# Kernel optimization log

Measured on AMD Instinct MI355X. Metric: run time of the kernel, lower is better.

Reference implementation:

```python
import jax, jax.numpy as jnp
import numpy as np

H = W = 256
L = H * W                      # number of graph vertices / tree leaves
N_NODES = 2 * L - 1            # binary partition tree node count
LAM = 1.0                      # lambda_ (soft-area temperature)


def _grid_edges():
    """4-adjacency grid graph edges (same structure as higra get_4_adjacency_graph)."""
    idx = np.arange(L, dtype=np.int64).reshape(H, W)
    src = np.concatenate([idx[:, :-1].ravel(), idx[:-1, :].ravel()])
    dst = np.concatenate([idx[:, 1:].ravel(), idx[1:, :].ravel()])
    return src.astype(np.int32), dst.astype(np.int32)


def setup_inputs() -> dict:
    key = jax.random.key(0)
    src, dst = _grid_edges()
    ew = jax.random.uniform(key, (src.shape[0],), dtype=jnp.float32)
    return {"edge_weights": ew,
            "edges_src": jnp.asarray(src),
            "edges_dst": jnp.asarray(dst)}


def _build_tree(ew, src, dst):
    """higra.bpt_canonical: Kruskal over stably-sorted edges, building a binary
    merge tree. Leaves are 0..L-1, internal node L+i is created by the i-th MST
    edge. Returns (sizes, mst_edge_map, ancestor paths). All integer structure
    is piecewise-constant w.r.t. edge_weights (no gradient flows through it)."""
    order = np.argsort(ew, kind="stable")
    uf = np.arange(L)

    def find(x):
        r = x
        while uf[r] != r:
            r = uf[r]
        while uf[x] != r:
            uf[x], x = r, uf[x]
        return r

    canon = np.arange(L)                      # tree node of each union-find root
    parent = np.arange(N_NODES)               # self-parent until set (root keeps self)
    sizes = np.ones(N_NODES, dtype=np.float32)
    edge_map = np.zeros(L - 1, dtype=np.int64)
    node = L
    for ei in order:
        a = find(src[ei]); b = find(dst[ei])
        if a == b:
            continue
        na, nb = canon[a], canon[b]
        parent[na] = node
        parent[nb] = node
        sizes[node] = sizes[na] + sizes[nb]
        edge_map[node - L] = ei
        uf[a] = b
        canon[b] = node
        node += 1
    # self-inclusive ancestor paths, padded by repeating the root
    cur = np.arange(N_NODES)
    cols = [cur.copy()]
    while np.any(parent[cur] != cur):
        cur = parent[cur]
        cols.append(cur.copy())
    paths = np.stack(cols, axis=1)            # [N_NODES, D+1]
    return sizes, edge_map, paths


def _softarea(edge_weights, edge_map, sizes_np, paths_np):
    """Soft area of every tree node n:
       area(n) = sum_x sigmoid((alt(n) - d(x, n)) / lambda)
    where d(x,n) is the min ultrametric distance from leaf x to the leaves of n:
      - x in subtree(n), x != n : d = alt(parent(x))
      - x == n (leaf)           : d = 0
      - x outside subtree(n)    : d = alt(lowest ancestor of n containing x).
    Outside leaves are grouped per ancestor a (count = size(a) - size(previous
    node on the path)), giving an O(N * depth) vectorized computation."""
    alt = jnp.concatenate([jnp.zeros((L,), edge_weights.dtype),
                           edge_weights[edge_map]])          # [N_NODES]
    alt_path = alt[paths_np]                                  # [N, D+1]
    size_path = sizes_np[paths_np]                            # constant, numpy
    diff = jnp.asarray(size_path[:, 1:] - size_path[:, :-1])  # 0 on root padding
    outside = jnp.sum(
        diff * jax.nn.sigmoid((alt[:, None] - alt_path[:, 1:]) / LAM), axis=1)

    # inside: each leaf x contributes sigmoid((alt(a_k) - alt(parent(x)))/lam)
    # to every proper ancestor a_k, plus sigmoid(0)=0.5 to itself (alt(leaf)=0).
    lp = paths_np[:L]                                         # [L, D+1]
    alt_lp = alt_path[:L]
    valid = jnp.asarray((lp[:, 1:] != lp[:, :-1]).astype(np.float32))
    vals = jax.nn.sigmoid((alt_lp[:, 1:] - alt_lp[:, 1:2]) / LAM) * valid
    inside = jax.ops.segment_sum(vals.reshape(-1),
                                 jnp.asarray(lp[:, 1:].reshape(-1)),
                                 num_segments=N_NODES)
    inside = inside.at[:L].add(0.5)
    return inside + outside


def reference(edge_weights, edges_src, edges_dst):
    sizes, edge_map, paths = _build_tree(np.asarray(edge_weights),
                                         np.asarray(edges_src),
                                         np.asarray(edges_dst))
    return _softarea(edge_weights, jnp.asarray(edge_map), sizes, paths)
```

## Files before the change

kernel.cpp:

```cpp
#include <hip/hip_runtime.h>
#include <stdint.h>

typedef unsigned int u32;
typedef unsigned short u16;

#define L_VERTS 65536
#define N_EDGES 130560
#define N_NODES 131071
#define NODEPAD 131072

#define CCH 170
#define SCH 768
#define MAXSV 1536
#define HSZ 2048

#define NB 255
#define TPB 64
#define IPT 8
#define IPB 512

__global__ void init_keys(const float* __restrict__ w, u32* __restrict__ keys, u32* __restrict__ vals,
                          u32* szG, u16* canonTop16, u32* parent, float* alt){
  int i = blockIdx.x*blockDim.x + threadIdx.x;
  if(i < N_EDGES){ keys[i] = __float_as_uint(w[i]); vals[i] = (u32)i; }
  if(i < N_NODES){ parent[i]=(u32)i; alt[i]=0.f; }
  if(i < L_VERTS){ szG[i]=1u; canonTop16[i]=0xFFFFu; }
}

__global__ void radix_hist(const u32* __restrict__ idx, const u32* __restrict__ keys,
                           u32* __restrict__ histG, int shift){
  __shared__ u32 h[256];
  for(int i=threadIdx.x;i<256;i+=TPB) h[i]=0;
  __syncthreads();
  int base = blockIdx.x*IPB + threadIdx.x*IPT;
  #pragma unroll
  for(int i=0;i<IPT;i++){
    u32 e = idx[base+i];
    u32 d = (keys[e]>>shift)&255u;
    atomicAdd(&h[d],1u);
  }
  __syncthreads();
  for(int i=threadIdx.x;i<256;i+=TPB) histG[i*NB+blockIdx.x]=h[i];
}

__global__ void radix_scan(u32* histG){
  const int M = 256*NB;
  __shared__ u32 sums[1024];
  int t=threadIdx.x; int s=t*64; u32 acc=0;
  for(int i=0;i<64;i++){int id=s+i; if(id<M) acc+=histG[id];}
  sums[t]=acc; __syncthreads();
  for(int off=1; off<1024; off<<=1){
    u32 v=(t>=off)?sums[t-off]:0u;
    __syncthreads();
    sums[t]+=v;
    __syncthreads();
  }
  u32 run = (t==0)?0u:sums[t-1];
  for(int i=0;i<64;i++){int id=s+i; if(id<M){u32 v=histG[id]; histG[id]=run; run+=v;}}
}

__global__ void radix_scatter(const u32* __restrict__ idxIn, const u32* __restrict__ keys,
                              u32* __restrict__ idxOut, const u32* __restrict__ histG, int shift){
  __shared__ u16 thoff[256][TPB];
  int t=threadIdx.x;
  for(int d=t;d<256;d+=TPB) for(int j=0;j<TPB;j++) thoff[d][j]=0;
  __syncthreads();
  int base = blockIdx.x*IPB + t*IPT;
  u32 myv[IPT]; u32 myd[IPT];
  #pragma unroll
  for(int i=0;i<IPT;i++){
    myv[i]=idxIn[base+i];
    myd[i]=(keys[myv[i]]>>shift)&255u;
    thoff[myd[i]][t]++;
  }
  __syncthreads();
  for(int dd=0;dd<4;dd++){
    int d=t*4+dd; u32 run=0;
    for(int j=0;j<TPB;j++){ u32 v=thoff[d][j]; thoff[d][j]=(u16)run; run+=v; }
  }
  __syncthreads();
  #pragma unroll
  for(int i=0;i<IPT;i++){
    u32 d=myd[i];
    u32 pos = histG[d*NB+blockIdx.x] + (u32)thoff[d][t];
    thoff[d][t]++;
    idxOut[pos]=myv[i];
  }
}

__global__ void build_epair(const u32* __restrict__ order, const int* __restrict__ srcv,
                            const int* __restrict__ dstv, u32* __restrict__ epair){
  int p=blockIdx.x*blockDim.x+threadIdx.x;
  if(p>=N_EDGES) return;
  u32 e=order[p];
  epair[p]=((u32)dstv[e]<<16)|(u32)srcv[e];
}

__device__ __forceinline__ u32 ald(u32* p){
  return __hip_atomic_load(p, __ATOMIC_RELAXED, __HIP_MEMORY_SCOPE_AGENT);
}
__device__ __forceinline__ void ast(u32* p, u32 v){
  __hip_atomic_store(p, v, __ATOMIC_RELAXED, __HIP_MEMORY_SCOPE_AGENT);
}

__global__ void __launch_bounds__(1024,1) p1_checkpoints(
    const u32* __restrict__ epair,
    u32* szG, u16* lid16, u16* svroot16, u16* svsize16, u16* svnext16, u32* mG)
{
  __shared__ u16 ufL[L_VERTS];
  __shared__ u32 hkey[HSZ];
  __shared__ u32 sufL[MAXSV];
  __shared__ u32 compsz[MAXSV];
  __shared__ u32 repkey[MAXSV];
  __shared__ u16 lidL[2*SCH];
  __shared__ u32 mcnt;
  int t = threadIdx.x;
  for(int i=t;i<L_VERTS/2;i+=1024) ((u32*)ufL)[i]=((2u*(u32)i+1u)<<16)|(2u*(u32)i);
  for(int k=0;k<CCH;k++){
    for(int i=t;i<HSZ;i+=1024) hkey[i]=0xFFFFFFFFu;
    for(u32 s=t;s<MAXSV;s+=1024){ sufL[s]=s; compsz[s]=0u; repkey[s]=0u; }
    if(t==0) mcnt=0u;
    __syncthreads();
    int base = k*SCH;
    for(int i=t;i<2*SCH;i+=1024){
      u32 pr = epair[base+(i>>1)];
      u32 v = (i&1)? (pr>>16) : (pr&0xFFFFu);
      u32 x=v;
      while(true){ u32 px=ufL[x]; if(px==x)break; u32 g=ufL[px]; if(g!=px) ufL[x]=(u16)g; x=g; }
      u32 r=x;
      if(v!=r) ufL[v]=(u16)r;
      u32 h=(r*2654435761u)>>21;
      while(true){
        u32 old=atomicCAS(&hkey[h],0xFFFFFFFFu,(r<<16)|0x7FFFu);
        if(old==0xFFFFFFFFu){
          u32 id=atomicAdd(&mcnt,1u);
          svroot16[k*MAXSV+id]=(u16)r;
          hkey[h]=(r<<16)|id;
          break;
        }
        if((old>>16)==r) break;
        h=(h+1)&(HSZ-1u);
      }
      lidL[i]=(u16)h;
    }
    __syncthreads();
    u32 mc=mcnt;
    if(t==0) mG[k]=mc;
    for(u32 s=t;s<mc;s+=1024){
      u32 r=(u32)svroot16[k*MAXSV+s];
      svsize16[k*MAXSV+s]=(u16)(ald(&szG[r])-1u);
    }
    for(int i=t;i<2*SCH;i+=1024) lid16[2*base+i]=(u16)(hkey[lidL[i]]&0xFFFFu);
    for(int j=t;j<SCH;j+=1024){
      u32 sa=hkey[lidL[2*j]]&0xFFFFu, sb=hkey[lidL[2*j+1]]&0xFFFFu;
      if(sa==sb) continue;
      while(true){
        u32 x=sa; while(true){u32 p2=sufL[x]; if(p2==x)break; u32 g=sufL[p2]; if(g!=p2) sufL[x]=g; x=g;}
        u32 y=sb; while(true){u32 p2=sufL[y]; if(p2==y)break; u32 g=sufL[p2]; if(g!=p2) sufL[y]=g; y=g;}
        if(x==y) break;
        u32 hi=x>y?x:y, lo=x^y^hi;
        if(atomicCAS(&sufL[hi],hi,lo)==hi) break;
        sa=hi; sb=lo;
      }
    }
    __syncthreads();
    for(u32 s=t;s<mc;s+=1024){
      u32 x=s; while(true){u32 p2=sufL[x]; if(p2==x)break; x=p2;}
      sufL[s]=x;
      u32 sz=(u32)svsize16[k*MAXSV+s]+1u;
      atomicAdd(&compsz[x], sz);
      atomicMax(&repkey[x], (sz<<11) | (2047u-s));
    }
    __syncthreads();
    for(u32 s=t;s<mc;s+=1024){
      u32 rs=sufL[s];
      u32 rep=2047u-(repkey[rs]&2047u);
      u32 wv=(u32)svroot16[k*MAXSV+rep];
      svnext16[k*MAXSV+s]=(u16)wv;
      u32 myroot=(u32)svroot16[k*MAXSV+s];
      if(myroot!=wv) ufL[myroot]=(u16)wv;
      if(s==rep)     ast(&szG[wv], compsz[rs]);
    }
    __syncthreads();
  }
}

__global__ void __launch_bounds__(64) p2_chunk(
  const u16* __restrict__ lid16,
  const u16* __restrict__ svsize16, const u16* __restrict__ svnext16, const u32* __restrict__ mG,
  u16* __restrict__ outChA, u16* __restrict__ outChB, u16* __restrict__ outSize16, u16* __restrict__ outJ16,
  u32* __restrict__ accCnt, u16* __restrict__ compR16, u16* __restrict__ compTop16, u32* __restrict__ ncomp)
{
  int k = blockIdx.x; int t = threadIdx.x;
  __shared__ u16 uf[MAXSV];
  __shared__ u32 csize[MAXSV];
  __shared__ u16 ctop[MAXSV];
  __shared__ u16 svnl[MAXSV];
  __shared__ u32 lidP[SCH];
  __shared__ u32 cmp_s;
  u32 m = mG[k];
  int base=k*SCH;
  for(u32 s=t;s<m;s+=64){
    uf[s]=(u16)s;
    csize[s]=(u32)svsize16[k*MAXSV+s]+1u;
    ctop[s]=(u16)s;
    svnl[s]=svnext16[k*MAXSV+s];
  }
  for(int j=t;j<SCH;j+=64) lidP[j]=((const u32*)lid16)[base+j];
  if(t==0) cmp_s=0u;
  __syncthreads();
  if(t==0){
    u32 cnt=0;
    for(int j=0;j<SCH;j++){
      u32 lw = lidP[j];
      u32 la = lw & 0xFFFFu, lb = lw >> 16;
      u32 x=la; while(true){u32 px=uf[x]; if(px==x)break; u32 g=uf[px]; uf[x]=(u16)g; x=g;}
      u32 y=lb; while(true){u32 py=uf[y]; if(py==y)break; u32 g=uf[py]; uf[y]=(u16)g; y=g;}
      if(x==y) continue;
      u32 sa=csize[x], sb=csize[y], ns=sa+sb;
      outChA[base+cnt]=ctop[x];
      outChB[base+cnt]=ctop[y];
      outSize16[base+cnt]=(u16)(ns-1u);
      outJ16[base+cnt]=(u16)j;
      u32 win=(sa>=sb)?x:y, los=x^y^win;
      uf[los]=(u16)win; csize[win]=ns; ctop[win]=(u16)(0x8000u|cnt);
      cnt++;
    }
    accCnt[k]=cnt;
  }
  __syncthreads();
  for(u32 s=t;s<m;s+=64){
    if(uf[s]==(u16)s && (ctop[s]&0x8000u)){
      u32 pos=atomicAdd(&cmp_s,1u);
      compR16[k*MAXSV+pos]=svnl[s];
      compTop16[k*MAXSV+pos]=(u16)(ctop[s]&0x7FFFu);
    }
  }
  __syncthreads();
  if(t==0) ncomp[k]=cmp_s;
}

__global__ void __launch_bounds__(1024) p3_stitch(
  const u32* __restrict__ accCnt, const u16* __restrict__ outChA, const u16* __restrict__ outChB,
  const u16* __restrict__ outSize16, const u16* __restrict__ outJ16,
  const u16* __restrict__ svroot16,
  const u16* __restrict__ compR16, const u16* __restrict__ compTop16, const u32* __restrict__ ncomp,
  const u32* __restrict__ order, const float* __restrict__ w,
  u16* __restrict__ canonTop16, u32* __restrict__ parent, float* __restrict__ alt, u16* __restrict__ usize16)
{
  __shared__ u32 accBase[CCH];
  int t=threadIdx.x;
  if(t==0){ u32 r=0; for(int k=0;k<CCH;k++){ accBase[k]=r; r+=accCnt[k]; } }
  __syncthreads();
  for(int idx=t; idx<N_EDGES; idx+=1024){
    int k = idx/SCH; int j = idx - k*SCH;
    if(j < (int)accCnt[k]){
      u32 nid = (u32)L_VERTS + accBase[k] + (u32)j;
      u32 p = (u32)(k*SCH) + (u32)outJ16[idx];
      alt[nid] = w[order[p]];
      usize16[nid] = outSize16[idx];
      u32 cA=outChA[idx]; if(cA & 0x8000u) parent[(u32)L_VERTS+accBase[k]+(cA&0x7FFFu)] = nid;
      u32 cB=outChB[idx]; if(cB & 0x8000u) parent[(u32)L_VERTS+accBase[k]+(cB&0x7FFFu)] = nid;
    }
  }
  __syncthreads();
  for(int k=0;k<CCH;k++){
    u32 ac=accCnt[k];
    for(u32 j=t;j<ac;j+=1024){
      u32 idx=(u32)(k*SCH)+j;
      u32 nid=(u32)L_VERTS+accBase[k]+j;
      u32 cA=outChA[idx];
      if(!(cA&0x8000u)){
        u32 root=(u32)svroot16[k*MAXSV+cA];
        u32 ct=(u32)canonTop16[root];
        parent[(ct==0xFFFFu)?root:((u32)L_VERTS+ct)]=nid;
      }
      u32 cB=outChB[idx];
      if(!(cB&0x8000u)){
        u32 root=(u32)svroot16[k*MAXSV+cB];
        u32 ct=(u32)canonTop16[root];
        parent[(ct==0xFFFFu)?root:((u32)L_VERTS+ct)]=nid;
      }
    }
    __syncthreads();
    u32 nc=ncomp[k];
    for(u32 j=t;j<nc;j+=1024){
      canonTop16[(u32)compR16[k*MAXSV+j]] = (u16)(accBase[k]+compTop16[k*MAXSV+j]);
    }
    __syncthreads();
  }
}

__device__ __forceinline__ void hvals6(float v, float* o){
  float v2=v*v, v3=v2*v, v4=v2*v2, v5=v4*v;
  o[0]=0.5f-0.25f*v+v3*(1.f/48.f)-v5*(1.f/480.f);
  o[1]=0.25f-v2*(1.f/16.f)+v4*(1.f/96.f);
  o[2]=v*(1.f/16.f)-v3*(1.f/48.f);
  o[3]=v2*(1.f/48.f)-(1.f/48.f);
  o[4]=-v*(1.f/96.f);
  o[5]=(1.f/480.f);
}

__global__ void zero_both(u32* cc, float* nodeM, u32* ctr){
  int i=blockIdx.x*blockDim.x+threadIdx.x;
  if(i<L_VERTS) cc[i]=0u;
  if(i<6*NODEPAD) nodeM[i]=0.f;
  if(i==0) *ctr=0u;
}

__global__ void prep_init(const u32* __restrict__ parent, const u16* __restrict__ usize16,
                          u32* cc, u32* J0, uint2* A0, float* out){
  int n=blockIdx.x*blockDim.x+threadIdx.x;
  if(n>=N_NODES) return;
  out[n] = (n<L_VERTS)?0.5f:0.0f;
  if(n==N_NODES-1){ J0[n]=(u32)n; A0[n]=make_uint2(0u,0u); return; }
  u32 p=parent[n];
  u32 ord=atomicAdd(&cc[p-L_VERTS],1u);
  u32 szP=(u32)usize16[p]+1u;
  u32 szN=(n<L_VERTS)?1u:((u32)usize16[n]+1u);
  u32 sib=szP-szN;
  A0[n]=make_uint2(ord? sib:0u, 1u + (ord? (2u*sib-1u):0u));
  J0[n]=p;
}

__global__ void triple_round(const u32* __restrict__ Jin, const uint2* __restrict__ Ain,
                             u32* __restrict__ Jout, uint2* __restrict__ Aout){
  int n=blockIdx.x*blockDim.x+threadIdx.x;
  if(n>=N_NODES) return;
  u32 j1=Jin[n], j2=Jin[j1], j3=Jin[j2], j4=Jin[j3], j5=Jin[j4], j6=Jin[j5], j7=Jin[j6];
  uint2 a0=Ain[n], a1=Ain[j1], a2=Ain[j2], a3=Ain[j3], a4=Ain[j4], a5=Ain[j5], a6=Ain[j6], a7=Ain[j7];
  Aout[n]=make_uint2(a0.x+a1.x+a2.x+a3.x+a4.x+a5.x+a6.x+a7.x,
                     a0.y+a1.y+a2.y+a3.y+a4.y+a5.y+a6.y+a7.y);
  Jout[n]=Jin[j7];
}

__global__ void scatter_all(const u32* __restrict__ parent, const float* __restrict__ alt,
                            const u16* __restrict__ usize16, const uint2* __restrict__ accF,
                            float* __restrict__ leafM, float* __restrict__ nodeM){
  int n=blockIdx.x*blockDim.x+threadIdx.x;
  if(n>=N_NODES) return;
  u32 p=parent[n];
  float h[6]; hvals6(alt[p],h);
  uint2 af=accF[n];
  if(n<L_VERTS){
    u32 pos=af.x;
    #pragma unroll
    for(int j=0;j<6;j++) leafM[(size_t)j*L_VERTS+pos]=h[j];
  }
  if(n<N_NODES-1){
    u32 szP=(u32)usize16[p]+1u;
    u32 szN=(n<L_VERTS)?1u:((u32)usize16[n]+1u);
    float d=(float)(szP-szN);
    u32 q0=af.y;
    u32 q1=q0 + 2u*szN - 1u;
    #pragma unroll
    for(int j=0;j<6;j++){
      float tm=d*h[j];
      atomicAdd(&nodeM[(size_t)j*NODEPAD+q0], tm);
      atomicAdd(&nodeM[(size_t)j*NODEPAD+q1], -tm);
    }
  }
}

__global__ void scanAll(float* __restrict__ leafM, float* __restrict__ nodeM,
                        float* __restrict__ bsumL, float* __restrict__ bsumN, u32* ctr){
  int b=blockIdx.x; int t=threadIdx.x;
  float* arr; u32 base; float* bs;
  if(b<6*64){ int row=b>>6, blk=b&63;  arr=leafM+(size_t)row*L_VERTS;  base=(u32)blk*1024u; bs=&bsumL[row*64+blk]; }
  else      { int bb=b-384; int row=bb>>7, blk=bb&127; arr=nodeM+(size_t)row*NODEPAD; base=(u32)blk*1024u; bs=&bsumN[row*128+blk]; }
  __shared__ float s[256];
  __shared__ u32 lastFlag;
  base += (u32)t*4u;
  float v0=arr[base],v1=arr[base+1],v2=arr[base+2],v3=arr[base+3];
  v1+=v0; v2+=v1; v3+=v2;
  s[t]=v3; __syncthreads();
  for(int o=1;o<256;o<<=1){ float x=(t>=o)?s[t-o]:0.f; __syncthreads(); s[t]+=x; __syncthreads(); }
  float pre=(t>0)?s[t-1]:0.f;
  arr[base]=v0+pre; arr[base+1]=v1+pre; arr[base+2]=v2+pre; arr[base+3]=v3+pre;
  if(t==255) *bs=s[255];
  __threadfence();
  if(t==0) lastFlag = (atomicAdd(ctr,1u)==1151u) ? 1u : 0u;
  __syncthreads();
  if(lastFlag){
    __threadfence();
    if(t<6){ float r=0; for(int i=0;i<64;i++){ float v=bsumL[t*64+i]; bsumL[t*64+i]=r; r+=v; } }
    else if(t<12){ int j=t-6; float r=0; for(int i=0;i<128;i++){ float v=bsumN[j*128+i]; bsumN[j*128+i]=r; r+=v; } }
  }
}

__global__ void eval_all(const uint2* __restrict__ accF, const float* __restrict__ alt,
                         const u16* __restrict__ usize16, const float* __restrict__ leafM,
                         const float* __restrict__ nodeM, const float* __restrict__ bsumL,
                         const float* __restrict__ bsumN, float* __restrict__ out){
  int n=blockIdx.x*blockDim.x+threadIdx.x;
  if(n>=N_NODES) return;
  uint2 af=accF[n];
  float u=alt[n];
  u32 q=af.y;
  float acc=0.f, up=1.f;
  #pragma unroll
  for(int j=0;j<6;j++){
    float T = nodeM[(size_t)j*NODEPAD+q] + bsumN[j*128 + (q>>10)];
    acc += up*T;
    up*=u;
  }
  if(n>=L_VERTS){
    u32 lo=af.x;
    u32 hi=lo + (u32)usize16[n] + 1u;
    up=1.f;
    #pragma unroll
    for(int j=0;j<6;j++){
      const float* arr=leafM + (size_t)j*L_VERTS;
      const float* bs=bsumL + j*64;
      float Ph = arr[hi-1u] + bs[(hi-1u)>>10];
      float Pl = lo ? (arr[lo-1u] + bs[(lo-1u)>>10]) : 0.f;
      acc += up*(Ph-Pl);
      up*=u;
    }
  }
  out[n]+=acc;
}

__global__ void ws_too_small(float* out){
  int i=blockIdx.x*blockDim.x+threadIdx.x;
  if(i<N_NODES) out[i]=1.0e6f;
}

extern "C" void kernel_launch(void* const* d_in, const int* in_sizes, int n_in,
                              void* d_out, int out_size, void* d_ws, size_t ws_size,
                              hipStream_t stream){
  (void)in_sizes; (void)n_in; (void)out_size;
  const float* w  = (const float*)d_in[0];
  const int* src  = (const int*)d_in[1];
  const int* dst  = (const int*)d_in[2];
  float* out = (float*)d_out;

  char* ws = (char*)d_ws;
  size_t off=0;
  auto alloc=[&](size_t bytes)->void*{ void* p = ws+off; off += (bytes+511)&~(size_t)511; return p; };
  u32* parent   =(u32*)alloc((size_t)N_NODES*4);
  float* alt    =(float*)alloc((size_t)N_NODES*4);
  u16* usize16  =(u16*)alloc((size_t)N_NODES*2);
  float* bsumL  =(float*)alloc(6*64*4);
  float* bsumN  =(float*)alloc(6*128*4);
  u32* ctr      =(u32*)alloc(512);
  size_t scratch0=off;
  u32* keys0    =(u32*)alloc((size_t)N_EDGES*4);
  u32* vals0    =(u32*)alloc((size_t)N_EDGES*4);
  u32* vals1    =(u32*)alloc((size_t)N_EDGES*4);
  u32* histG    =(u32*)alloc(256*NB*4);
  u16* canonTop16=(u16*)alloc((size_t)L_VERTS*2);
  u16* outJ16   =(u16*)alloc((size_t)N_EDGES*2);
  u16* svroot16 =(u16*)alloc((size_t)CCH*MAXSV*2);
  u16* svsize16 =(u16*)alloc((size_t)CCH*MAXSV*2);
  u16* svnext16 =(u16*)alloc((size_t)CCH*MAXSV*2);
  u32* mG       =(u32*)alloc(CCH*4);
  u32* accCnt   =(u32*)alloc(CCH*4);
  u32* ncomp    =(u32*)alloc(CCH*4);
  size_t endA=off;
  off=scratch0;
  u32* ccChsum  =(u32*)alloc((size_t)L_VERTS*4);
  u32* J0       =(u32*)alloc((size_t)N_NODES*4);
  u32* J1       =(u32*)alloc((size_t)N_NODES*4);
  uint2* A0     =(uint2*)alloc((size_t)N_NODES*8);
  uint2* A1     =(uint2*)alloc((size_t)N_NODES*8);
  float* nodeM  =(float*)alloc((size_t)6*NODEPAD*4);
  size_t endB=off;
  float* leafM  =(float*)ccChsum;

  if((endA>ws_size)||(endB>ws_size)){
    ws_too_small<<<(N_NODES+255)/256,256,0,stream>>>(out);
    return;
  }

  u16* lid16    =(u16*)vals1;
  u32* epair    =keys0;
  u16* outChA16 =(u16*)histG;
  u16* outChB16 =(u16*)keys0;
  u16* outSize16=(u16*)((char*)keys0 + (size_t)N_EDGES*2);
  u16* compR16  =svsize16;
  u16* compTop16=svnext16;
  u32* szG      =(u32*)usize16;

  init_keys<<<(N_NODES+255)/256,256,0,stream>>>(w,keys0,vals0,szG,canonTop16,parent,alt);
  for(int pass=0;pass<4;pass++){
    const u32* iv = (pass&1)?vals1:vals0;
    u32* ov = (pass&1)?vals0:vals1;
    int shift=pass*8;
    radix_hist   <<<NB,TPB,0,stream>>>(iv,keys0,histG,shift);
    radix_scan   <<<1,1024,0,stream>>>(histG);
    radix_scatter<<<NB,TPB,0,stream>>>(iv,keys0,ov,histG,shift);
  }
  build_epair<<<(N_EDGES+255)/256,256,0,stream>>>(vals0,src,dst,epair);
  p1_checkpoints<<<1,1024,0,stream>>>(epair,szG,lid16,svroot16,svsize16,svnext16,mG);
  p2_chunk<<<CCH,64,0,stream>>>(lid16,svsize16,svnext16,mG,
                                outChA16,outChB16,outSize16,outJ16,accCnt,compR16,compTop16,ncomp);
  p3_stitch<<<1,1024,0,stream>>>(accCnt,outChA16,outChB16,outSize16,outJ16,svroot16,
                                 compR16,compTop16,ncomp,vals0,w,canonTop16,parent,alt,usize16);
  zero_both<<<(6*NODEPAD+255)/256,256,0,stream>>>(ccChsum,nodeM,ctr);
  prep_init<<<(N_NODES+255)/256,256,0,stream>>>(parent,usize16,ccChsum,J1,A1,out);
  for(int r=0;r<6;r++){
    if((r&1)==0) triple_round<<<(N_NODES+255)/256,256,0,stream>>>(J1,A1,J0,A0);
    else         triple_round<<<(N_NODES+255)/256,256,0,stream>>>(J0,A0,J1,A1);
  }
  const uint2* accF=A1;
  scatter_all<<<(N_NODES+255)/256,256,0,stream>>>(parent,alt,usize16,accF,leafM,nodeM);
  scanAll<<<1152,256,0,stream>>>(leafM,nodeM,bsumL,bsumN,ctr);
  eval_all<<<(N_NODES+255)/256,256,0,stream>>>(accF,alt,usize16,leafM,nodeM,bsumL,bsumN,out);
}
```

Before: 2.916 ms.

## Fuse checkpoint, chunk and stitch phases into one pipelined kernel

Merges the three tree-build kernels into a single launch. Block 0 runs the sequential checkpoint pass and then the stitch, while the other blocks each wait on a global progress flag and process their chunk as soon as its checkpoint is published. The per-chunk sequential union-find work now overlaps with the checkpoint loop instead of running after it, and two kernel launches are removed. In exchange it relies on inter-block spin-waiting with acquire/release atomics, which needs all 171 blocks co-resident to avoid deadlock. The chunk blocks now launch 1024 threads where the old chunk kernel used 64, and the size output moves to its own buffer.

```diff
diff --git a/kernel.cpp b/kernel.cpp
--- a/kernel.cpp
+++ b/kernel.cpp
@@ -20,11 +20,12 @@
 #define IPB 512
 
 __global__ void init_keys(const float* __restrict__ w, u32* __restrict__ keys, u32* __restrict__ vals,
-                          u32* szG, u16* canonTop16, u32* parent, float* alt){
+                          u32* szG, u16* canonTop16, u32* parent, float* alt, u32* ctr){
   int i = blockIdx.x*blockDim.x + threadIdx.x;
   if(i < N_EDGES){ keys[i] = __float_as_uint(w[i]); vals[i] = (u32)i; }
   if(i < N_NODES){ parent[i]=(u32)i; alt[i]=0.f; }
   if(i < L_VERTS){ szG[i]=1u; canonTop16[i]=0xFFFFu; }
+  if(i < 4) ctr[i]=0u;
 }
 
 __global__ void radix_hist(const u32* __restrict__ idx, const u32* __restrict__ keys,
@@ -103,191 +104,198 @@
   __hip_atomic_store(p, v, __ATOMIC_RELAXED, __HIP_MEMORY_SCOPE_AGENT);
 }
 
-__global__ void __launch_bounds__(1024,1) p1_checkpoints(
+__global__ void __launch_bounds__(1024,1) build_fused(
     const u32* __restrict__ epair,
-    u32* szG, u16* lid16, u16* svroot16, u16* svsize16, u16* svnext16, u32* mG)
+    u32* szG, u16* lid16, u16* svroot16, u16* svsize16, u16* svnext16, u32* mG,
+    u16* outChA, u16* outChB, u16* outS16, u16* outJ16,
+    u32* accCnt, u16* compR16, u16* compTop16, u32* ncomp,
+    const u32* __restrict__ order, const float* __restrict__ w,
+    u16* canonTop16, u32* parent, float* alt, u16* usize16,
+    u32* flagChunk, u32* doneCnt)
 {
-  __shared__ u16 ufL[L_VERTS];
-  __shared__ u32 hkey[HSZ];
-  __shared__ u32 sufL[MAXSV];
-  __shared__ u32 compsz[MAXSV];
-  __shared__ u32 repkey[MAXSV];
-  __shared__ u16 lidL[2*SCH];
-  __shared__ u32 mcnt;
+  __shared__ char pool[160840] __attribute__((aligned(16)));
   int t = threadIdx.x;
-  for(int i=t;i<L_VERTS/2;i+=1024) ((u32*)ufL)[i]=((2u*(u32)i+1u)<<16)|(2u*(u32)i);
-  for(int k=0;k<CCH;k++){
-    for(int i=t;i<HSZ;i+=1024) hkey[i]=0xFFFFFFFFu;
-    for(u32 s=t;s<MAXSV;s+=1024){ sufL[s]=s; compsz[s]=0u; repkey[s]=0u; }
-    if(t==0) mcnt=0u;
-    __syncthreads();
-    int base = k*SCH;
-    for(int i=t;i<2*SCH;i+=1024){
-      u32 pr = epair[base+(i>>1)];
-      u32 v = (i&1)? (pr>>16) : (pr&0xFFFFu);
-      u32 x=v;
-      while(true){ u32 px=ufL[x]; if(px==x)break; u32 g=ufL[px]; if(g!=px) ufL[x]=(u16)g; x=g; }
-      u32 r=x;
-      if(v!=r) ufL[v]=(u16)r;
-      u32 h=(r*2654435761u)>>21;
-      while(true){
-        u32 old=atomicCAS(&hkey[h],0xFFFFFFFFu,(r<<16)|0x7FFFu);
-        if(old==0xFFFFFFFFu){
-          u32 id=atomicAdd(&mcnt,1u);
-          svroot16[k*MAXSV+id]=(u16)r;
-          hkey[h]=(r<<16)|id;
-          break;
+  if(blockIdx.x==0){
+    u16* ufL   =(u16*)pool;
+    u32* hkey  =(u32*)(pool+131072);
+    u32* sufL  =(u32*)(pool+139264);
+    u32* compsz=(u32*)(pool+145408);
+    u32* repkey=(u32*)(pool+151552);
+    u16* lidL  =(u16*)(pool+157696);
+    u32* mcntp =(u32*)(pool+160768);
+    for(int i=t;i<L_VERTS/2;i+=1024) ((u32*)ufL)[i]=((2u*(u32)i+1u)<<16)|(2u*(u32)i);
+    for(int k=0;k<CCH;k++){
+      for(int i=t;i<HSZ;i+=1024) hkey[i]=0xFFFFFFFFu;
+      for(u32 s=t;s<MAXSV;s+=1024){ sufL[s]=s; compsz[s]=0u; repkey[s]=0u; }
+      if(t==0) *mcntp=0u;
+      __syncthreads();
+      int base = k*SCH;
+      for(int i=t;i<2*SCH;i+=1024){
+        u32 pr = epair[base+(i>>1)];
+        u32 v = (i&1)? (pr>>16) : (pr&0xFFFFu);
+        u32 x=v;
+        while(true){ u32 px=ufL[x]; if(px==x)break; u32 g=ufL[px]; if(g!=px) ufL[x]=(u16)g; x=g; }
+        u32 r=x;
+        if(v!=r) ufL[v]=(u16)r;
+        u32 h=(r*2654435761u)>>21;
+        while(true){
+          u32 old=atomicCAS(&hkey[h],0xFFFFFFFFu,(r<<16)|0x7FFFu);
+          if(old==0xFFFFFFFFu){
+            u32 id=atomicAdd(mcntp,1u);
+            svroot16[k*MAXSV+id]=(u16)r;
+            hkey[h]=(r<<16)|id;
+            break;
+          }
+          if((old>>16)==r) break;
+          h=(h+1)&(HSZ-1u);
         }
-        if((old>>16)==r) break;
-        h=(h+1)&(HSZ-1u);
-      }
-      lidL[i]=(u16)h;
-    }
-    __syncthreads();
-    u32 mc=mcnt;
-    if(t==0) mG[k]=mc;
-    for(u32 s=t;s<mc;s+=1024){
-      u32 r=(u32)svroot16[k*MAXSV+s];
-      svsize16[k*MAXSV+s]=(u16)(ald(&szG[r])-1u);
-    }
-    for(int i=t;i<2*SCH;i+=1024) lid16[2*base+i]=(u16)(hkey[lidL[i]]&0xFFFFu);
-    for(int j=t;j<SCH;j+=1024){
-      u32 sa=hkey[lidL[2*j]]&0xFFFFu, sb=hkey[lidL[2*j+1]]&0xFFFFu;
-      if(sa==sb) continue;
-      while(true){
-        u32 x=sa; while(true){u32 p2=sufL[x]; if(p2==x)break; u32 g=sufL[p2]; if(g!=p2) sufL[x]=g; x=g;}
-        u32 y=sb; while(true){u32 p2=sufL[y]; if(p2==y)break; u32 g=sufL[p2]; if(g!=p2) sufL[y]=g; y=g;}
-        if(x==y) break;
-        u32 hi=x>y?x:y, lo=x^y^hi;
-        if(atomicCAS(&sufL[hi],hi,lo)==hi) break;
-        sa=hi; sb=lo;
-      }
-    }
-    __syncthreads();
-    for(u32 s=t;s<mc;s+=1024){
-      u32 x=s; while(true){u32 p2=sufL[x]; if(p2==x)break; x=p2;}
-      sufL[s]=x;
-      u32 sz=(u32)svsize16[k*MAXSV+s]+1u;
-      atomicAdd(&compsz[x], sz);
-      atomicMax(&repkey[x], (sz<<11) | (2047u-s));
-    }
-    __syncthreads();
-    for(u32 s=t;s<mc;s+=1024){
-      u32 rs=sufL[s];
-      u32 rep=2047u-(repkey[rs]&2047u);
-      u32 wv=(u32)svroot16[k*MAXSV+rep];
-      svnext16[k*MAXSV+s]=(u16)wv;
-      u32 myroot=(u32)svroot16[k*MAXSV+s];
-      if(myroot!=wv) ufL[myroot]=(u16)wv;
-      if(s==rep)     ast(&szG[wv], compsz[rs]);
-    }
-    __syncthreads();
-  }
-}
-
-__global__ void __launch_bounds__(64) p2_chunk(
-  const u16* __restrict__ lid16,
-  const u16* __restrict__ svsize16, const u16* __restrict__ svnext16, const u32* __restrict__ mG,
-  u16* __restrict__ outChA, u16* __restrict__ outChB, u16* __restrict__ outSize16, u16* __restrict__ outJ16,
-  u32* __restrict__ accCnt, u16* __restrict__ compR16, u16* __restrict__ compTop16, u32* __restrict__ ncomp)
-{
-  int k = blockIdx.x; int t = threadIdx.x;
-  __shared__ u16 uf[MAXSV];
-  __shared__ u32 csize[MAXSV];
-  __shared__ u16 ctop[MAXSV];
-  __shared__ u16 svnl[MAXSV];
-  __shared__ u32 lidP[SCH];
-  __shared__ u32 cmp_s;
-  u32 m = mG[k];
-  int base=k*SCH;
-  for(u32 s=t;s<m;s+=64){
-    uf[s]=(u16)s;
-    csize[s]=(u32)svsize16[k*MAXSV+s]+1u;
-    ctop[s]=(u16)s;
-    svnl[s]=svnext16[k*MAXSV+s];
-  }
-  for(int j=t;j<SCH;j+=64) lidP[j]=((const u32*)lid16)[base+j];
-  if(t==0) cmp_s=0u;
-  __syncthreads();
-  if(t==0){
-    u32 cnt=0;
-    for(int j=0;j<SCH;j++){
-      u32 lw = lidP[j];
-      u32 la = lw & 0xFFFFu, lb = lw >> 16;
-      u32 x=la; while(true){u32 px=uf[x]; if(px==x)break; u32 g=uf[px]; uf[x]=(u16)g; x=g;}
-      u32 y=lb; while(true){u32 py=uf[y]; if(py==y)break; u32 g=uf[py]; uf[y]=(u16)g; y=g;}
-      if(x==y) continue;
-      u32 sa=csize[x], sb=csize[y], ns=sa+sb;
-      outChA[base+cnt]=ctop[x];
-      outChB[base+cnt]=ctop[y];
-      outSize16[base+cnt]=(u16)(ns-1u);
-      outJ16[base+cnt]=(u16)j;
-      u32 win=(sa>=sb)?x:y, los=x^y^win;
-      uf[los]=(u16)win; csize[win]=ns; ctop[win]=(u16)(0x8000u|cnt);
-      cnt++;
-    }
-    accCnt[k]=cnt;
-  }
-  __syncthreads();
-  for(u32 s=t;s<m;s+=64){
-    if(uf[s]==(u16)s && (ctop[s]&0x8000u)){
-      u32 pos=atomicAdd(&cmp_s,1u);
-      compR16[k*MAXSV+pos]=svnl[s];
-      compTop16[k*MAXSV+pos]=(u16)(ctop[s]&0x7FFFu);
-    }
-  }
-  __syncthreads();
-  if(t==0) ncomp[k]=cmp_s;
-}
-
-__global__ void __launch_bounds__(1024) p3_stitch(
-  const u32* __restrict__ accCnt, const u16* __restrict__ outChA, const u16* __restrict__ outChB,
-  const u16* __restrict__ outSize16, const u16* __restrict__ outJ16,
-  const u16* __restrict__ svroot16,
-  const u16* __restrict__ compR16, const u16* __restrict__ compTop16, const u32* __restrict__ ncomp,
-  const u32* __restrict__ order, const float* __restrict__ w,
-  u16* __restrict__ canonTop16, u32* __restrict__ parent, float* __restrict__ alt, u16* __restrict__ usize16)
-{
-  __shared__ u32 accBase[CCH];
-  int t=threadIdx.x;
-  if(t==0){ u32 r=0; for(int k=0;k<CCH;k++){ accBase[k]=r; r+=accCnt[k]; } }
-  __syncthreads();
-  for(int idx=t; idx<N_EDGES; idx+=1024){
-    int k = idx/SCH; int j = idx - k*SCH;
-    if(j < (int)accCnt[k]){
-      u32 nid = (u32)L_VERTS + accBase[k] + (u32)j;
-      u32 p = (u32)(k*SCH) + (u32)outJ16[idx];
-      alt[nid] = w[order[p]];
-      usize16[nid] = outSize16[idx];
-      u32 cA=outChA[idx]; if(cA & 0x8000u) parent[(u32)L_VERTS+accBase[k]+(cA&0x7FFFu)] = nid;
-      u32 cB=outChB[idx]; if(cB & 0x8000u) parent[(u32)L_VERTS+accBase[k]+(cB&0x7FFFu)] = nid;
-    }
-  }
-  __syncthreads();
-  for(int k=0;k<CCH;k++){
-    u32 ac=accCnt[k];
-    for(u32 j=t;j<ac;j+=1024){
-      u32 idx=(u32)(k*SCH)+j;
-      u32 nid=(u32)L_VERTS+accBase[k]+j;
-      u32 cA=outChA[idx];
-      if(!(cA&0x8000u)){
-        u32 root=(u32)svroot16[k*MAXSV+cA];
-        u32 ct=(u32)canonTop16[root];
-        parent[(ct==0xFFFFu)?root:((u32)L_VERTS+ct)]=nid;
-      }
-      u32 cB=outChB[idx];
-      if(!(cB&0x8000u)){
-        u32 root=(u32)svroot16[k*MAXSV+cB];
-        u32 ct=(u32)canonTop16[root];
-        parent[(ct==0xFFFFu)?root:((u32)L_VERTS+ct)]=nid;
-      }
-    }
-    __syncthreads();
-    u32 nc=ncomp[k];
-    for(u32 j=t;j<nc;j+=1024){
-      canonTop16[(u32)compR16[k*MAXSV+j]] = (u16)(accBase[k]+compTop16[k*MAXSV+j]);
-    }
-    __syncthreads();
+        lidL[i]=(u16)h;
+      }
+      __syncthreads();
+      u32 mc=*mcntp;
+      if(t==0) mG[k]=mc;
+      for(u32 s=t;s<mc;s+=1024){
+        u32 r=(u32)svroot16[k*MAXSV+s];
+        svsize16[k*MAXSV+s]=(u16)(ald(&szG[r])-1u);
+      }
+      for(int i=t;i<2*SCH;i+=1024) lid16[2*base+i]=(u16)(hkey[lidL[i]]&0xFFFFu);
+      for(int j=t;j<SCH;j+=1024){
+        u32 sa=hkey[lidL[2*j]]&0xFFFFu, sb=hkey[lidL[2*j+1]]&0xFFFFu;
+        if(sa==sb) continue;
+        while(true){
+          u32 x=sa; while(true){u32 p2=sufL[x]; if(p2==x)break; u32 g=sufL[p2]; if(g!=p2) sufL[x]=g; x=g;}
+          u32 y=sb; while(true){u32 p2=sufL[y]; if(p2==y)break; u32 g=sufL[p2]; if(g!=p2) sufL[y]=g; y=g;}
+          if(x==y) break;
+          u32 hi=x>y?x:y, lo=x^y^hi;
+          if(atomicCAS(&sufL[hi],hi,lo)==hi) break;
+          sa=hi; sb=lo;
+        }
+      }
+      __syncthreads();
+      for(u32 s=t;s<mc;s+=1024){
+        u32 x=s; while(true){u32 p2=sufL[x]; if(p2==x)break; x=p2;}
+        sufL[s]=x;
+        u32 sz=(u32)svsize16[k*MAXSV+s]+1u;
+        atomicAdd(&compsz[x], sz);
+        atomicMax(&repkey[x], (sz<<11) | (2047u-s));
+      }
+      __syncthreads();
+      for(u32 s=t;s<mc;s+=1024){
+        u32 rs=sufL[s];
+        u32 rep=2047u-(repkey[rs]&2047u);
+        u32 wv=(u32)svroot16[k*MAXSV+rep];
+        svnext16[k*MAXSV+s]=(u16)wv;
+        u32 myroot=(u32)svroot16[k*MAXSV+s];
+        if(myroot!=wv) ufL[myroot]=(u16)wv;
+        if(s==rep)     ast(&szG[wv], compsz[rs]);
+      }
+      __syncthreads();
+      if(t==0) __hip_atomic_store(flagChunk,(u32)(k+1),__ATOMIC_RELEASE,__HIP_MEMORY_SCOPE_AGENT);
+    }
+    if(t==0){
+      while(__hip_atomic_load(doneCnt,__ATOMIC_ACQUIRE,__HIP_MEMORY_SCOPE_AGENT)<(u32)CCH)
+        __builtin_amdgcn_s_sleep(2);
+      __threadfence();
+    }
+    __syncthreads();
+    u32* accBase=(u32*)pool;
+    if(t==0){ u32 r=0; for(int k=0;k<CCH;k++){ accBase[k]=r; r+=accCnt[k]; } }
+    __syncthreads();
+    for(int idx=t; idx<N_EDGES; idx+=1024){
+      int k = idx/SCH; int j = idx - k*SCH;
+      if(j < (int)accCnt[k]){
+        u32 nid = (u32)L_VERTS + accBase[k] + (u32)j;
+        u32 p = (u32)(k*SCH) + (u32)outJ16[idx];
+        alt[nid] = w[order[p]];
+        usize16[nid] = outS16[idx];
+        u32 cA=outChA[idx]; if(cA & 0x8000u) parent[(u32)L_VERTS+accBase[k]+(cA&0x7FFFu)] = nid;
+        u32 cB=outChB[idx]; if(cB & 0x8000u) parent[(u32)L_VERTS+accBase[k]+(cB&0x7FFFu)] = nid;
+      }
+    }
+    __syncthreads();
+    for(int k=0;k<CCH;k++){
+      u32 ac=accCnt[k];
+      for(u32 j=t;j<ac;j+=1024){
+        u32 idx=(u32)(k*SCH)+j;
+        u32 nid=(u32)L_VERTS+accBase[k]+j;
+        u32 cA=outChA[idx];
+        if(!(cA&0x8000u)){
+          u32 root=(u32)svroot16[k*MAXSV+cA];
+          u32 ct=(u32)canonTop16[root];
+          parent[(ct==0xFFFFu)?root:((u32)L_VERTS+ct)]=nid;
+        }
+        u32 cB=outChB[idx];
+        if(!(cB&0x8000u)){
+          u32 root=(u32)svroot16[k*MAXSV+cB];
+          u32 ct=(u32)canonTop16[root];
+          parent[(ct==0xFFFFu)?root:((u32)L_VERTS+ct)]=nid;
+        }
+      }
+      __syncthreads();
+      u32 nc=ncomp[k];
+      for(u32 j=t;j<nc;j+=1024){
+        canonTop16[(u32)compR16[k*MAXSV+j]] = (u16)(accBase[k]+compTop16[k*MAXSV+j]);
+      }
+      __syncthreads();
+    }
+  } else {
+    int k = blockIdx.x-1;
+    u16* uf   =(u16*)pool;
+    u32* csize=(u32*)(pool+3072);
+    u16* ctop =(u16*)(pool+9216);
+    u16* svnl =(u16*)(pool+12288);
+    u32* lidP =(u32*)(pool+15360);
+    u32* cmp_p=(u32*)(pool+18432);
+    if(t==0){
+      while(__hip_atomic_load(flagChunk,__ATOMIC_ACQUIRE,__HIP_MEMORY_SCOPE_AGENT) < (u32)(k+1))
+        __builtin_amdgcn_s_sleep(2);
+      __threadfence();
+    }
+    __syncthreads();
+    u32 m = mG[k];
+    int base=k*SCH;
+    for(u32 s=t;s<m;s+=1024){
+      uf[s]=(u16)s;
+      csize[s]=(u32)svsize16[k*MAXSV+s]+1u;
+      ctop[s]=(u16)s;
+      svnl[s]=svnext16[k*MAXSV+s];
+    }
+    for(int j=t;j<SCH;j+=1024) lidP[j]=((const u32*)lid16)[base+j];
+    if(t==0) *cmp_p=0u;
+    __syncthreads();
+    if(t==0){
+      u32 cnt=0;
+      for(int j=0;j<SCH;j++){
+        u32 lw = lidP[j];
+        u32 la = lw & 0xFFFFu, lb = lw >> 16;
+        u32 x=la; while(true){u32 px=uf[x]; if(px==x)break; u32 g=uf[px]; uf[x]=(u16)g; x=g;}
+        u32 y=lb; while(true){u32 py=uf[y]; if(py==y)break; u32 g=uf[py]; uf[y]=(u16)g; y=g;}
+        if(x==y) continue;
+        u32 sa=csize[x], sb=csize[y], ns=sa+sb;
+        outChA[base+cnt]=ctop[x];
+        outChB[base+cnt]=ctop[y];
+        outS16[base+cnt]=(u16)(ns-1u);
+        outJ16[base+cnt]=(u16)j;
+        u32 win=(sa>=sb)?x:y, los=x^y^win;
+        uf[los]=(u16)win; csize[win]=ns; ctop[win]=(u16)(0x8000u|cnt);
+        cnt++;
+      }
+      accCnt[k]=cnt;
+    }
+    __syncthreads();
+    for(u32 s=t;s<m;s+=1024){
+      if(uf[s]==(u16)s && (ctop[s]&0x8000u)){
+        u32 pos=atomicAdd(cmp_p,1u);
+        compR16[k*MAXSV+pos]=svnl[s];
+        compTop16[k*MAXSV+pos]=(u16)(ctop[s]&0x7FFFu);
+      }
+    }
+    __syncthreads();
+    if(t==0){
+      ncomp[k]=*cmp_p;
+      __threadfence();
+      __hip_atomic_fetch_add(doneCnt,1u,__ATOMIC_RELEASE,__HIP_MEMORY_SCOPE_AGENT);
+    }
   }
 }
 
@@ -451,6 +459,7 @@
   u32* histG    =(u32*)alloc(256*NB*4);
   u16* canonTop16=(u16*)alloc((size_t)L_VERTS*2);
   u16* outJ16   =(u16*)alloc((size_t)N_EDGES*2);
+  u16* outS16   =(u16*)alloc((size_t)N_EDGES*2);
   u16* svroot16 =(u16*)alloc((size_t)CCH*MAXSV*2);
   u16* svsize16 =(u16*)alloc((size_t)CCH*MAXSV*2);
   u16* svnext16 =(u16*)alloc((size_t)CCH*MAXSV*2);
@@ -477,12 +486,13 @@
   u32* epair    =keys0;
   u16* outChA16 =(u16*)histG;
   u16* outChB16 =(u16*)keys0;
-  u16* outSize16=(u16*)((char*)keys0 + (size_t)N_EDGES*2);
   u16* compR16  =svsize16;
   u16* compTop16=svnext16;
   u32* szG      =(u32*)usize16;
-
-  init_keys<<<(N_NODES+255)/256,256,0,stream>>>(w,keys0,vals0,szG,canonTop16,parent,alt);
+  u32* flagChunk=&ctr[1];
+  u32* doneCnt  =&ctr[2];
+
+  init_keys<<<(N_NODES+255)/256,256,0,stream>>>(w,keys0,vals0,szG,canonTop16,parent,alt,ctr);
   for(int pass=0;pass<4;pass++){
     const u32* iv = (pass&1)?vals1:vals0;
     u32* ov = (pass&1)?vals0:vals1;
@@ -492,12 +502,12 @@
     radix_scatter<<<NB,TPB,0,stream>>>(iv,keys0,ov,histG,shift);
   }
   build_epair<<<(N_EDGES+255)/256,256,0,stream>>>(vals0,src,dst,epair);
-  p1_checkpoints<<<1,1024,0,stream>>>(epair,szG,lid16,svroot16,svsize16,svnext16,mG);
-  p2_chunk<<<CCH,64,0,stream>>>(lid16,svsize16,svnext16,mG,
-                                outChA16,outChB16,outSize16,outJ16,accCnt,compR16,compTop16,ncomp);
-  p3_stitch<<<1,1024,0,stream>>>(accCnt,outChA16,outChB16,outSize16,outJ16,svroot16,
-                                 compR16,compTop16,ncomp,vals0,w,canonTop16,parent,alt,usize16);
-  zero_both<<<(6*NODEPAD+255)/256,256,0,stream>>>(ccChsum,nodeM,ctr);
+  build_fused<<<CCH+1,1024,0,stream>>>(epair,szG,lid16,svroot16,svsize16,svnext16,mG,
+                                       outChA16,outChB16,outS16,outJ16,
+                                       accCnt,compR16,compTop16,ncomp,
+                                       vals0,w,canonTop16,parent,alt,usize16,
+                                       flagChunk,doneCnt);
+  zero_both<<<(6*NODEPAD+255)/256,256,0,stream>>>(ccChsum,nodeM,&ctr[0]);
   prep_init<<<(N_NODES+255)/256,256,0,stream>>>(parent,usize16,ccChsum,J1,A1,out);
   for(int r=0;r<6;r++){
     if((r&1)==0) triple_round<<<(N_NODES+255)/256,256,0,stream>>>(J1,A1,J0,A0);
@@ -505,6 +515,6 @@
   }
   const uint2* accF=A1;
   scatter_all<<<(N_NODES+255)/256,256,0,stream>>>(parent,alt,usize16,accF,leafM,nodeM);
-  scanAll<<<1152,256,0,stream>>>(leafM,nodeM,bsumL,bsumN,ctr);
+  scanAll<<<1152,256,0,stream>>>(leafM,nodeM,bsumL,bsumN,&ctr[0]);
   eval_all<<<(N_NODES+255)/256,256,0,stream>>>(accF,alt,usize16,leafM,nodeM,bsumL,bsumN,out);
 }
```

Result: slower. 3.894 ms (+33.5%).
